# Performance work log

Hardware: AMD Instinct MI355X
Metric: run time of the kernel (lower is better)

The kernel has to match this reference:

```python
import jax, jax.numpy as jnp
import numpy as np

T = 2.0  # __init__ arg t (temperature exponent); logits scaled by exp(t)


def setup_inputs() -> dict:
    key = jax.random.key(0)
    k1, k2 = jax.random.split(key)
    N = 4096
    logits_per_image = jax.random.normal(k1, (N, N), dtype=jnp.float32)
    labels = jax.random.randint(k2, (N,), 0, 512, dtype=jnp.int64)
    return {"logits_per_image": logits_per_image, "labels": labels}


def reference(logits_per_image, labels):
    # p[i,j] = softmax over row i of (logits * exp(t))
    N = logits_per_image.shape[0]
    p = jax.nn.softmax(logits_per_image * jnp.exp(jnp.float32(T)), axis=1)
    # mask[i,j] = 1 iff i==j or labels[i] != labels[j]; loss uses
    #   log p[i,i] on the diagonal, mask * log(1 - p[i,j]) off-diagonal.
    diag_term = jnp.sum(jnp.log(jnp.diagonal(p)))
    neq = (labels[:, None] != labels[None, :]).astype(p.dtype)  # zero on diagonal
    off_term = jnp.sum(neq * jnp.log1p(-p))
    return (diag_term + off_term) / N
```

## Files before the change

### kernel.cpp

```cpp
#include <hip/hip_runtime.h>

#define N_DIM 4096
#define SCALE 7.3890560989306495f

__global__ __launch_bounds__(256, 4) void minfonce_kernel(
    const float* __restrict__ logits,
    const int*   __restrict__ labels,
    float*       __restrict__ out)
{
    const int tid  = threadIdx.x;
    const int lane = tid & 63;
    const int wv   = tid >> 6;
    const int half = wv & 1;
    const int row  = (blockIdx.x << 1) + (wv >> 1);

    __shared__ float sS[4], sX[4], sM[4], sA[4];

    const float4* rp = reinterpret_cast<const float4*>(logits + (size_t)row * N_DIM);
    const int4*   lp = reinterpret_cast<const int4*>(labels);
    const int     li = labels[row];
    const int     i0 = lane + (half << 9);

    const float4 u0 = rp[i0 +   0]; const int4 b0 = lp[i0 +   0];
    const float4 u1 = rp[i0 +  64]; const int4 b1 = lp[i0 +  64];
    const float4 u2 = rp[i0 + 128]; const int4 b2 = lp[i0 + 128];
    const float4 u3 = rp[i0 + 192]; const int4 b3 = lp[i0 + 192];
    const float4 u4 = rp[i0 + 256]; const int4 b4 = lp[i0 + 256];
    const float4 u5 = rp[i0 + 320]; const int4 b5 = lp[i0 + 320];
    const float4 u6 = rp[i0 + 384]; const int4 b6 = lp[i0 + 384];
    const float4 u7 = rp[i0 + 448]; const int4 b7 = lp[i0 + 448];
    __builtin_amdgcn_sched_barrier(0);

    float m8[8];
    float s_all = 0.f, s_mask = 0.f;
#define ACCG(G, T, B) do {                                             \
        const float ex = __expf(SCALE * T.x);                          \
        const float ey = __expf(SCALE * T.y);                          \
        const float ez = __expf(SCALE * T.z);                          \
        const float ew = __expf(SCALE * T.w);                          \
        s_all  += (ex + ey) + (ez + ew);                               \
        s_mask += ((B.x != li ? ex : 0.f) + (B.y != li ? ey : 0.f))    \
                + ((B.z != li ? ez : 0.f) + (B.w != li ? ew : 0.f));   \
        m8[G] = fmaxf(fmaxf(ex, ey), fmaxf(ez, ew));                   \
    } while (0)
    ACCG(0, u0, b0); ACCG(1, u1, b1); ACCG(2, u2, b2); ACCG(3, u3, b3);
    ACCG(4, u4, b4); ACCG(5, u5, b5); ACCG(6, u6, b6); ACCG(7, u7, b7);
#undef ACCG

    float emax = m8[0];
#pragma unroll
    for (int g = 1; g < 8; ++g) emax = fmaxf(emax, m8[g]);

#pragma unroll
    for (int off = 1; off < 64; off <<= 1) {
        s_all  += __shfl_xor(s_all, off);
        s_mask += __shfl_xor(s_mask, off);
        emax    = fmaxf(emax, __shfl_xor(emax, off));
    }
    if (lane == 0) { sS[wv] = s_all; sX[wv] = s_mask; sM[wv] = emax; }
    __syncthreads();

    const int   w0    = wv & ~1;
    const float S     = sS[w0] + sS[w0 | 1];
    const float Smask = sX[w0] + sX[w0 | 1];
    const float Emax  = fmaxf(sM[w0], sM[w0 | 1]);
    const float invS  = 1.0f / S;
    const float tau   = 1e-3f * S;
    const float qmax  = fmaxf(S - Emax, S * 1e-12f) * invS;

    float acc = 0.f;
#define FIX1(X, L) {                                                   \
        const float ev = __expf(SCALE * (X));                          \
        if (ev > tau && (L) != li) {                                   \
            const float p = ev * invS;                                 \
            const float q = (ev == Emax) ? qmax : (1.0f - p);          \
            acc += __logf(q) + p; } }
#define FIXG(G, T, B) if (m8[G] > tau) {                               \
        FIX1(T.x, B.x) FIX1(T.y, B.y) FIX1(T.z, B.z) FIX1(T.w, B.w) }
    FIXG(0, u0, b0); FIXG(1, u1, b1); FIXG(2, u2, b2); FIXG(3, u3, b3);
    FIXG(4, u4, b4); FIXG(5, u5, b5); FIXG(6, u6, b6); FIXG(7, u7, b7);
#undef FIXG
#undef FIX1

    if (half == 0 && lane == 0)
        acc += (SCALE * logits[(size_t)row * N_DIM + row] - __logf(S))
             - Smask * invS;

#pragma unroll
    for (int off = 1; off < 64; off <<= 1)
        acc += __shfl_xor(acc, off);

    if (lane == 0) sA[wv] = acc;
    __syncthreads();
    if (tid == 0) {
        const float total = (sA[0] + sA[1]) + (sA[2] + sA[3]);
        atomicAdd(out, total * (1.0f / N_DIM));
    }
}

extern "C" void kernel_launch(void* const* d_in, const int* in_sizes, int n_in,
                              void* d_out, int out_size, void* d_ws, size_t ws_size,
                              hipStream_t stream) {
    const float* logits = (const float*)d_in[0];
    const int*   labels = (const int*)d_in[1];
    float*       out    = (float*)d_out;

    hipMemsetAsync(out, 0, sizeof(float), stream);
    minfonce_kernel<<<N_DIM / 2, 256, 0, stream>>>(logits, labels, out);
}
```

Baseline: 115.2 us.

## Stage labels in LDS, process four rows per block, replace atomic with reduce kernel

Each 512-thread block now loads the full label vector into shared memory once and serves four rows from it, instead of every wave pulling the labels from global memory. The diagonal load is issued up front, and the fix-up pass re-reads row data instead of holding it in registers. The final sum is written per block to a workspace and added up by a small second kernel, replacing the memset and global atomic. Costs are an extra kernel launch, a 16KB LDS allocation that may limit occupancy, and possible re-fetch of logits in the fix-up pass.

```diff
diff --git a/kernel.cpp b/kernel.cpp
--- a/kernel.cpp
+++ b/kernel.cpp
@@ -3,48 +3,55 @@
 #define N_DIM 4096
 #define SCALE 7.3890560989306495f
 
-__global__ __launch_bounds__(256, 4) void minfonce_kernel(
+__global__ __launch_bounds__(512, 8) void minfonce_rows(
     const float* __restrict__ logits,
     const int*   __restrict__ labels,
-    float*       __restrict__ out)
+    float*       __restrict__ ws)
 {
     const int tid  = threadIdx.x;
     const int lane = tid & 63;
     const int wv   = tid >> 6;
     const int half = wv & 1;
-    const int row  = (blockIdx.x << 1) + (wv >> 1);
+    const int row  = (blockIdx.x << 2) + (wv >> 1);
 
-    __shared__ float sS[4], sX[4], sM[4], sA[4];
+    __shared__ int4  slab[N_DIM / 4];
+    __shared__ float sS[8], sX[8], sM[8], sA[8];
+
+    const int4* lp = reinterpret_cast<const int4*>(labels);
+    slab[tid]       = lp[tid];
+    slab[tid + 512] = lp[tid + 512];
+    __syncthreads();
+    const int li = reinterpret_cast<const int*>(slab)[row];
 
     const float4* rp = reinterpret_cast<const float4*>(logits + (size_t)row * N_DIM);
-    const int4*   lp = reinterpret_cast<const int4*>(labels);
-    const int     li = labels[row];
     const int     i0 = lane + (half << 9);
 
-    const float4 u0 = rp[i0 +   0]; const int4 b0 = lp[i0 +   0];
-    const float4 u1 = rp[i0 +  64]; const int4 b1 = lp[i0 +  64];
-    const float4 u2 = rp[i0 + 128]; const int4 b2 = lp[i0 + 128];
-    const float4 u3 = rp[i0 + 192]; const int4 b3 = lp[i0 + 192];
-    const float4 u4 = rp[i0 + 256]; const int4 b4 = lp[i0 + 256];
-    const float4 u5 = rp[i0 + 320]; const int4 b5 = lp[i0 + 320];
-    const float4 u6 = rp[i0 + 384]; const int4 b6 = lp[i0 + 384];
-    const float4 u7 = rp[i0 + 448]; const int4 b7 = lp[i0 + 448];
+    const float4 u0 = rp[i0 +   0];
+    const float4 u1 = rp[i0 +  64];
+    const float4 u2 = rp[i0 + 128];
+    const float4 u3 = rp[i0 + 192];
+    const float4 u4 = rp[i0 + 256];
+    const float4 u5 = rp[i0 + 320];
+    const float4 u6 = rp[i0 + 384];
+    const float4 u7 = rp[i0 + 448];
+    const float  dv = logits[(size_t)row * N_DIM + row];
     __builtin_amdgcn_sched_barrier(0);
 
     float m8[8];
     float s_all = 0.f, s_mask = 0.f;
-#define ACCG(G, T, B) do {                                             \
-        const float ex = __expf(SCALE * T.x);                          \
-        const float ey = __expf(SCALE * T.y);                          \
-        const float ez = __expf(SCALE * T.z);                          \
-        const float ew = __expf(SCALE * T.w);                          \
+#define ACCG(G, U) do {                                                \
+        const int4  lb = slab[i0 + 64 * (G)];                          \
+        const float ex = __expf(SCALE * U.x);                          \
+        const float ey = __expf(SCALE * U.y);                          \
+        const float ez = __expf(SCALE * U.z);                          \
+        const float ew = __expf(SCALE * U.w);                          \
         s_all  += (ex + ey) + (ez + ew);                               \
-        s_mask += ((B.x != li ? ex : 0.f) + (B.y != li ? ey : 0.f))    \
-                + ((B.z != li ? ez : 0.f) + (B.w != li ? ew : 0.f));   \
+        s_mask += ((lb.x != li ? ex : 0.f) + (lb.y != li ? ey : 0.f))  \
+                + ((lb.z != li ? ez : 0.f) + (lb.w != li ? ew : 0.f)); \
         m8[G] = fmaxf(fmaxf(ex, ey), fmaxf(ez, ew));                   \
     } while (0)
-    ACCG(0, u0, b0); ACCG(1, u1, b1); ACCG(2, u2, b2); ACCG(3, u3, b3);
-    ACCG(4, u4, b4); ACCG(5, u5, b5); ACCG(6, u6, b6); ACCG(7, u7, b7);
+    ACCG(0, u0); ACCG(1, u1); ACCG(2, u2); ACCG(3, u3);
+    ACCG(4, u4); ACCG(5, u5); ACCG(6, u6); ACCG(7, u7);
 #undef ACCG
 
     float emax = m8[0];
@@ -59,7 +66,6 @@
     }
     if (lane == 0) { sS[wv] = s_all; sX[wv] = s_mask; sM[wv] = emax; }
     __syncthreads();
-
     const int   w0    = wv & ~1;
     const float S     = sS[w0] + sS[w0 | 1];
     const float Smask = sX[w0] + sX[w0 | 1];
@@ -75,27 +81,44 @@
             const float p = ev * invS;                                 \
             const float q = (ev == Emax) ? qmax : (1.0f - p);          \
             acc += __logf(q) + p; } }
-#define FIXG(G, T, B) if (m8[G] > tau) {                               \
-        FIX1(T.x, B.x) FIX1(T.y, B.y) FIX1(T.z, B.z) FIX1(T.w, B.w) }
-    FIXG(0, u0, b0); FIXG(1, u1, b1); FIXG(2, u2, b2); FIXG(3, u3, b3);
-    FIXG(4, u4, b4); FIXG(5, u5, b5); FIXG(6, u6, b6); FIXG(7, u7, b7);
+#define FIXG(G) if (m8[G] > tau) {                                     \
+        const float4 t  = rp[i0 + 64 * (G)];                           \
+        const int4   lb = slab[i0 + 64 * (G)];                         \
+        FIX1(t.x, lb.x) FIX1(t.y, lb.y) FIX1(t.z, lb.z) FIX1(t.w, lb.w) }
+    FIXG(0); FIXG(1); FIXG(2); FIXG(3);
+    FIXG(4); FIXG(5); FIXG(6); FIXG(7);
 #undef FIXG
 #undef FIX1
-
-    if (half == 0 && lane == 0)
-        acc += (SCALE * logits[(size_t)row * N_DIM + row] - __logf(S))
-             - Smask * invS;
 
 #pragma unroll
     for (int off = 1; off < 64; off <<= 1)
         acc += __shfl_xor(acc, off);
-
-    if (lane == 0) sA[wv] = acc;
+    if (lane == 0) {
+        float a = acc;
+        if (half == 0)
+            a += (SCALE * dv - __logf(S)) - Smask * invS;
+        sA[wv] = a;
+    }
     __syncthreads();
     if (tid == 0) {
-        const float total = (sA[0] + sA[1]) + (sA[2] + sA[3]);
-        atomicAdd(out, total * (1.0f / N_DIM));
+        const float total = ((sA[0] + sA[1]) + (sA[2] + sA[3]))
+                          + ((sA[4] + sA[5]) + (sA[6] + sA[7]));
+        ws[blockIdx.x] = total;
     }
+}
+
+__global__ __launch_bounds__(64) void minfonce_reduce(
+    const float* __restrict__ ws,
+    float*       __restrict__ out)
+{
+    const int lane = threadIdx.x;
+    float a = 0.f;
+#pragma unroll
+    for (int i = 0; i < 16; ++i) a += ws[lane + 64 * i];
+#pragma unroll
+    for (int off = 1; off < 64; off <<= 1)
+        a += __shfl_xor(a, off);
+    if (lane == 0) out[0] = a * (1.0f / N_DIM);
 }
 
 extern "C" void kernel_launch(void* const* d_in, const int* in_sizes, int n_in,
@@ -104,7 +127,8 @@
     const float* logits = (const float*)d_in[0];
     const int*   labels = (const int*)d_in[1];
     float*       out    = (float*)d_out;
+    float*       ws     = (float*)d_ws;
 
-    hipMemsetAsync(out, 0, sizeof(float), stream);
-    minfonce_kernel<<<N_DIM / 2, 256, 0, stream>>>(logits, labels, out);
+    minfonce_rows<<<N_DIM / 4, 512, 0, stream>>>(logits, labels, ws);
+    minfonce_reduce<<<1, 64, 0, stream>>>(ws, out);
 }
```

Result: faster. 95.83 us (-16.8%).
